# Kernel optimization log

Hardware: AMD Instinct MI355X
Metric: run time of the kernel (lower is better)

The kernel has to match this reference:

```python
import jax, jax.numpy as jnp
import numpy as np

N, E, B, DIM, NF, EF, HID = 50000, 100000, 2000, 64, 14, 4, 128


def setup_inputs() -> dict:
    key = jax.random.key(0)
    ks = jax.random.split(key, 30)
    rn = lambda k, shape, scale: jax.random.normal(k, shape, jnp.float32) * scale
    inp = {}
    inp["x"] = rn(ks[0], (N, NF), 1.0)
    inp["edge_attr"] = jax.random.uniform(ks[1], (E, EF), jnp.float32)
    inp["edge_index"] = jax.random.randint(ks[2], (2, E), 0, N)
    # equal-size graphs: 25 nodes per graph, sorted segment ids
    inp["batch"] = (jnp.arange(N, dtype=jnp.int32) // (N // B)).astype(jnp.int32)
    inp["lin0_w"] = rn(ks[3], (DIM, NF), (1.0 / NF) ** 0.5)
    inp["lin0_b"] = jnp.zeros((DIM,), jnp.float32)
    inp["mlp_w1"] = rn(ks[4], (HID, EF), (1.0 / EF) ** 0.5)
    inp["mlp_b1"] = jnp.zeros((HID,), jnp.float32)
    inp["mlp_w2"] = rn(ks[5], (DIM * DIM, HID), (1.0 / HID) ** 0.5)
    inp["mlp_b2"] = jnp.zeros((DIM * DIM,), jnp.float32)
    inp["root"] = rn(ks[6], (DIM, DIM), (1.0 / DIM) ** 0.5)
    inp["conv_b"] = jnp.zeros((DIM,), jnp.float32)
    inp["gru_wih"] = rn(ks[7], (3 * DIM, DIM), (1.0 / DIM) ** 0.5)
    inp["gru_whh"] = rn(ks[8], (3 * DIM, DIM), (1.0 / DIM) ** 0.5)
    inp["gru_bih"] = jnp.zeros((3 * DIM,), jnp.float32)
    inp["gru_bhh"] = jnp.zeros((3 * DIM,), jnp.float32)
    inp["lstm_wih"] = rn(ks[9], (4 * DIM, 2 * DIM), (1.0 / (2 * DIM)) ** 0.5)
    inp["lstm_whh"] = rn(ks[10], (4 * DIM, DIM), (1.0 / DIM) ** 0.5)
    inp["lstm_bih"] = jnp.zeros((4 * DIM,), jnp.float32)
    inp["lstm_bhh"] = jnp.zeros((4 * DIM,), jnp.float32)
    inp["lin1_w"] = rn(ks[11], (DIM, 2 * DIM), (1.0 / (2 * DIM)) ** 0.5)
    inp["lin1_b"] = jnp.zeros((DIM,), jnp.float32)
    inp["lin2_w"] = rn(ks[12], (1, DIM), (1.0 / DIM) ** 0.5)
    inp["lin2_b"] = jnp.zeros((1,), jnp.float32)
    return inp


def _forward(x, edge_attr, edge_index, batch, lin0_w, lin0_b, mlp_w1, mlp_b1,
             mlp_w2, mlp_b2, root, conv_b, gru_wih, gru_whh, gru_bih, gru_bhh,
             lstm_wih, lstm_whh, lstm_bih, lstm_bhh, lin1_w, lin1_b, lin2_w, lin2_b):
    src, dst = edge_index[0], edge_index[1]
    n = x.shape[0]
    # edge MLP -> per-edge weight matrices [E, DIM, DIM]
    h_e = jax.nn.relu(edge_attr @ mlp_w1.T + mlp_b1)
    W_e = (h_e @ mlp_w2.T + mlp_b2).reshape(-1, DIM, DIM)
    deg = jnp.clip(jax.ops.segment_sum(jnp.ones_like(dst, jnp.float32), dst, n), 1.0)

    out = jax.nn.relu(x @ lin0_w.T + lin0_b)
    h = out  # GRU hidden (seq_len=1, 1 layer)
    for _ in range(3):
        msg = jnp.einsum('ei,eio->eo', out[src], W_e)  # per-edge matmul
        agg = jax.ops.segment_sum(msg, dst, n) / deg[:, None]  # scatter-mean
        m = jax.nn.relu(agg + out @ root + conv_b)  # NNConv: aggr + root + bias
        # GRU step
        gi = m @ gru_wih.T + gru_bih
        gh = h @ gru_whh.T + gru_bhh
        i_r, i_z, i_n = jnp.split(gi, 3, axis=-1)
        h_r, h_z, h_n = jnp.split(gh, 3, axis=-1)
        r = jax.nn.sigmoid(i_r + h_r)
        z = jax.nn.sigmoid(i_z + h_z)
        ng = jnp.tanh(i_n + r * h_n)
        h = (1.0 - z) * ng + z * h
        out = h

    # Set2Set pooling, 3 processing steps
    b = B
    qh = jnp.zeros((b, DIM), out.dtype)
    qc = jnp.zeros((b, DIM), out.dtype)
    q_star = jnp.zeros((b, 2 * DIM), out.dtype)
    for _ in range(3):
        gates = q_star @ lstm_wih.T + lstm_bih + qh @ lstm_whh.T + lstm_bhh
        gi_, gf_, gg_, go_ = jnp.split(gates, 4, axis=-1)
        qc = jax.nn.sigmoid(gf_) * qc + jax.nn.sigmoid(gi_) * jnp.tanh(gg_)
        qh = jax.nn.sigmoid(go_) * jnp.tanh(qc)
        q = qh
        e = jnp.sum(out * q[batch], axis=-1)  # [N]
        e_max = jax.ops.segment_max(e, batch, b)
        a = jnp.exp(e - e_max[batch])
        denom = jax.ops.segment_sum(a, batch, b)
        a = a / denom[batch]
        r_read = jax.ops.segment_sum(a[:, None] * out, batch, b)
        q_star = jnp.concatenate([q, r_read], axis=-1)

    y = jax.nn.relu(q_star @ lin1_w.T + lin1_b)
    y = y @ lin2_w.T + lin2_b
    return y.reshape(-1)


def reference(x, edge_attr, edge_index, batch, lin0_w, lin0_b, mlp_w1, mlp_b1,
              mlp_w2, mlp_b2, root, conv_b, gru_wih, gru_whh, gru_bih, gru_bhh,
              lstm_wih, lstm_whh, lstm_bih, lstm_bhh, lin1_w, lin1_b, lin2_w, lin2_b):
    return _forward(x, edge_attr, edge_index, batch, lin0_w, lin0_b, mlp_w1, mlp_b1,
                    mlp_w2, mlp_b2, root, conv_b, gru_wih, gru_whh, gru_bih, gru_bhh,
                    lstm_wih, lstm_whh, lstm_bih, lstm_bhh, lin1_w, lin1_b, lin2_w, lin2_b)
```

## Files before the change

kernel.cpp:

```cpp
#include <hip/hip_runtime.h>
#include <hip/hip_bf16.h>

#define NN 50000
#define EE 100000
#define BB 2000
#define DIM 64
#define NF 14
#define EF 4
#define HID 128
#define EPAD 100096

typedef __attribute__((ext_vector_type(8))) _Float16 half8;
typedef __attribute__((ext_vector_type(4))) _Float16 half4;
typedef __attribute__((ext_vector_type(4))) float floatx4;

__device__ __forceinline__ float rcp_fast(float x) { return __builtin_amdgcn_rcpf(x); }
__device__ __forceinline__ float sig_fast(float x) { return rcp_fast(1.f + __expf(-x)); }
__device__ __forceinline__ float tanh_fast(float x) {
    float e = __expf(2.f * x);
    return 1.f - 2.f * rcp_fast(e + 1.f);
}

__global__ void prep_fused_kernel(
    const float* __restrict__ x, const float* __restrict__ lin0_w,
    const float* __restrict__ lin0_b, float* __restrict__ hv,
    const float* __restrict__ ea, const float* __restrict__ w1,
    const float* __restrict__ b1, _Float16* __restrict__ he,
    const int* __restrict__ ei, float* __restrict__ deg,
    const float* __restrict__ w2, _Float16* __restrict__ W2rT,
    const float* __restrict__ lih, const float* __restrict__ lhh,
    const float* __restrict__ l1, float* __restrict__ lihT,
    float* __restrict__ lhhT, float* __restrict__ l1T,
    const float* __restrict__ root, const float* __restrict__ b2,
    const float* __restrict__ gwih, const float* __restrict__ gwhh,
    const float* __restrict__ gbih, const float* __restrict__ gbhh,
    _Float16* __restrict__ W1h, _Float16* __restrict__ W2h,
    float* __restrict__ fbias) {
    int t = blockIdx.x * 256 + threadIdx.x;

    {
        int el = t >> 4, hc = t & 15;
        if (el < EPAD) {
            half8 o8 = {0, 0, 0, 0, 0, 0, 0, 0};
            if (el < EE) {
                const float4 a = *(const float4*)(ea + (size_t)el * 4);
                #pragma unroll
                for (int j = 0; j < 8; j++) {
                    int h = hc * 8 + j;
                    const float4 w = *(const float4*)(w1 + h * 4);
                    float acc = fmaxf(b1[h] + a.x * w.x + a.y * w.y + a.z * w.z + a.w * w.w, 0.f);
                    o8[j] = (_Float16)acc;
                }
                if (hc == 0) atomicAdd(&deg[ei[EE + el]], 1.0f);
            }
            *(half8*)(he + (size_t)el * 128 + hc * 8) = o8;
        }
    }
    if (t < NN * 8) {
        int n = t >> 3, dc = t & 7;
        float xv[NF];
        #pragma unroll
        for (int f = 0; f < NF; f++) xv[f] = x[(size_t)n * NF + f];
        float o[8];
        #pragma unroll
        for (int j = 0; j < 8; j++) {
            int d = dc * 8 + j;
            float acc = lin0_b[d];
            #pragma unroll
            for (int f = 0; f < NF; f++) acc += xv[f] * lin0_w[d * NF + f];
            o[j] = fmaxf(acc, 0.f);
        }
        *(float4*)(hv + (size_t)n * 64 + dc * 8)     = make_float4(o[0], o[1], o[2], o[3]);
        *(float4*)(hv + (size_t)n * 64 + dc * 8 + 4) = make_float4(o[4], o[5], o[6], o[7]);
    }
    if (t < 64 * 1024) {
        int o = t >> 10, kc = t & 1023;
        int k0 = kc * 8, i = k0 >> 7, h0 = k0 & 127;
        const float* src = w2 + (size_t)(i * 64 + o) * 128 + h0;
        const float4 a = *(const float4*)src;
        const float4 b = *(const float4*)(src + 4);
        half8 r = {(_Float16)a.x, (_Float16)a.y, (_Float16)a.z, (_Float16)a.w,
                   (_Float16)b.x, (_Float16)b.y, (_Float16)b.z, (_Float16)b.w};
        *(half8*)(W2rT + (size_t)o * 8192 + k0) = r;
    }
    if (t < 256 * 128) { int j = t / 128, k = t % 128; lihT[k * 256 + j] = lih[t]; }
    if (t < 256 * 64) { int j = t / 64, k = t % 64; lhhT[k * 256 + j] = lhh[t]; }
    if (t < 64 * 128) { int d = t / 128, k = t % 128; l1T[k * 64 + d] = l1[t]; }
    if (t < 64 * 128) {
        int n = t >> 7, k = t & 127;
        W1h[t] = (_Float16)(k < 64 ? root[k * 64 + n] : b2[(size_t)(k - 64) * 64 + n]);
    }
    if (t < 256 * 128) {
        int n2 = t >> 7, k = t & 127;
        int g = n2 >> 6, j = n2 & 63;
        float v;
        if (g == 0)      v = (k < 64) ? gwih[j * 64 + k]         : gwhh[j * 64 + (k - 64)];
        else if (g == 1) v = (k < 64) ? gwih[(64 + j) * 64 + k]  : gwhh[(64 + j) * 64 + (k - 64)];
        else if (g == 2) v = (k < 64) ? gwih[(128 + j) * 64 + k] : 0.f;
        else             v = (k < 64) ? 0.f                      : gwhh[(128 + j) * 64 + (k - 64)];
        W2h[t] = (_Float16)v;
    }
    if (t < 256) {
        int g = t >> 6, j = t & 63;
        float v = (g == 0) ? gbih[j] + gbhh[j]
                : (g == 1) ? gbih[64 + j] + gbhh[64 + j]
                : (g == 2) ? gbih[128 + j] : gbhh[128 + j];
        fbias[t] = v;
    }
}

__global__ __launch_bounds__(256, 2) void msg_gemm_kernel(
    const float* __restrict__ hv, const _Float16* __restrict__ he16,
    const _Float16* __restrict__ W2rT, const int* __restrict__ ei,
    float* __restrict__ agg, float* __restrict__ xsum) {
    __shared__ _Float16 sB[2][16 * 64 * 8];
    __shared__ _Float16 sXs[256 * 68];
    __shared__ int sDst[256];
    const int t = threadIdx.x;
    const int tile = blockIdx.x >> 1;
    const int ki = blockIdx.x & 1;
    const int eb = tile * 256;
    const int base = ki * 32;
    const int lane = t & 63;
    const int w = t >> 6;
    const int col = lane & 15;
    const int quad = lane >> 4;

    if (t < 256) {
        int e = eb + t;
        sDst[t] = (e < EE) ? ei[EE + e] : 0;
    }
    if (ki == 0) {
        #pragma unroll 4
        for (int rep = 0; rep < 16; rep++) {
            int idx = rep * 256 + t;
            int el = idx >> 4, d4 = idx & 15;
            int e = eb + el;
            float4 v = {0.f, 0.f, 0.f, 0.f};
            if (e < EE) {
                int src = ei[e];
                v = *(const float4*)(hv + (size_t)src * 64 + d4 * 4);
            }
            half4 h4 = {(_Float16)v.x, (_Float16)v.y, (_Float16)v.z, (_Float16)v.w};
            *(half4*)&sXs[el * 68 + d4 * 4] = h4;
        }
    } else {
        #pragma unroll 4
        for (int rep = 0; rep < 8; rep++) {
            int idx = rep * 256 + t;
            int el = idx >> 3, d4 = 8 + (idx & 7);
            int e = eb + el;
            float4 v = {0.f, 0.f, 0.f, 0.f};
            if (e < EE) {
                int src = ei[e];
                v = *(const float4*)(hv + (size_t)src * 64 + d4 * 4);
            }
            half4 h4 = {(_Float16)v.x, (_Float16)v.y, (_Float16)v.z, (_Float16)v.w};
            *(half4*)&sXs[el * 68 + d4 * 4] = h4;
        }
    }

    half8 heReg[4][4];
    #pragma unroll
    for (int mt = 0; mt < 4; mt++) {
        int row = eb + w * 64 + mt * 16 + col;
        #pragma unroll
        for (int p = 0; p < 4; p++)
            heReg[mt][p] = *(const half8*)(he16 + (size_t)row * 128 + p * 32 + quad * 8);
    }

    floatx4 Cacc[4][4];
    #pragma unroll
    for (int mt = 0; mt < 4; mt++)
        #pragma unroll
        for (int nt = 0; nt < 4; nt++)
            Cacc[mt][nt] = (floatx4){0.f, 0.f, 0.f, 0.f};

    const size_t gbase = (size_t)(w * 16 + col) * 8192 + quad * 8;
    half8 pre[4];
    {
        #pragma unroll
        for (int rep = 0; rep < 4; rep++)
            pre[rep] = *(const half8*)(W2rT + gbase + (size_t)base * 128 + rep * 32);
        #pragma unroll
        for (int rep = 0; rep < 4; rep++)
            *(half8*)&sB[0][((w * 4 + rep) * 64 + lane) * 8] = pre[rep];
    }
    __syncthreads();

    #pragma unroll 1
    for (int ii = 0; ii < 32; ii++) {
        int buf = ii & 1;
        if (ii < 31) {
            #pragma unroll
            for (int rep = 0; rep < 4; rep++)
                pre[rep] = *(const half8*)(W2rT + gbase + (size_t)(base + ii + 1) * 128 + rep * 32);
        }
        _Float16 xsx[4];
        #pragma unroll
        for (int mt = 0; mt < 4; mt++)
            xsx[mt] = sXs[(w * 64 + mt * 16 + col) * 68 + base + ii];
        #pragma unroll
        for (int ks = 0; ks < 4; ks++) {
            half8 bfr[4];
            #pragma unroll
            for (int nt = 0; nt < 4; nt++)
                bfr[nt] = *(const half8*)&sB[buf][((nt * 4 + ks) * 64 + lane) * 8];
            #pragma unroll
            for (int mt = 0; mt < 4; mt++) {
                half8 afr = heReg[mt][ks] * xsx[mt];
                #pragma unroll
                for (int nt = 0; nt < 4; nt++)
                    Cacc[mt][nt] = __builtin_amdgcn_mfma_f32_16x16x32_f16(afr, bfr[nt], Cacc[mt][nt], 0, 0, 0);
            }
        }
        if (ii < 31) {
            #pragma unroll
            for (int rep = 0; rep < 4; rep++)
                *(half8*)&sB[buf ^ 1][((w * 4 + rep) * 64 + lane) * 8] = pre[rep];
        }
        __syncthreads();
    }

    #pragma unroll
    for (int mt = 0; mt < 4; mt++) {
        #pragma unroll
        for (int r = 0; r < 4; r++) {
            int el = w * 64 + mt * 16 + quad * 4 + r;
            if (eb + el < EE) {
                float* ap = agg + (size_t)sDst[el] * 64 + col;
                #pragma unroll
                for (int nt = 0; nt < 4; nt++)
                    atomicAdd(ap + nt * 16, Cacc[mt][nt][r]);
            }
        }
    }
    if (ki == 0) {
        #pragma unroll 4
        for (int rep = 0; rep < 64; rep++) {
            int idx = rep * 256 + t;
            int el = idx >> 6, d = idx & 63;
            if (eb + el < EE)
                atomicAdd(&xsum[(size_t)sDst[el] * 64 + d], (float)sXs[el * 68 + d]);
        }
    }
}

__global__ __launch_bounds__(256, 2) void node_fused_kernel(
    const float* __restrict__ hv_in, float* __restrict__ agg,
    float* __restrict__ xsum, const float* __restrict__ deg,
    const _Float16* __restrict__ W1h, const _Float16* __restrict__ W2h,
    const float* __restrict__ fbias, const float* __restrict__ cb,
    float* __restrict__ hv_out) {
    __shared__ _Float16 sA1[64 * 136];
    __shared__ _Float16 sA2[64 * 136];
    __shared__ float sH[64 * 68];
    __shared__ float sAgg[64 * 68];
    const int t = threadIdx.x;
    const int nb = blockIdx.x * 64;
    const int n = t >> 2, part = t & 3;
    {
        int gn = nb + n;
        bool valid = gn < NN;
        float inv = 1.f;
        if (valid) inv = 1.f / fmaxf(deg[gn], 1.f);
        #pragma unroll
        for (int c4 = 0; c4 < 4; c4++) {
            int d0 = part * 16 + c4 * 4;
            float4 hvv = {0.f, 0.f, 0.f, 0.f}, agv = {0.f, 0.f, 0.f, 0.f}, xsv = {0.f, 0.f, 0.f, 0.f};
            if (valid) {
                hvv = *(const float4*)(hv_in + (size_t)gn * 64 + d0);
                agv = *(const float4*)(agg + (size_t)gn * 64 + d0);
                xsv = *(const float4*)(xsum + (size_t)gn * 64 + d0);
            }
            agv.x *= inv; agv.y *= inv; agv.z *= inv; agv.w *= inv;
            xsv.x *= inv; xsv.y *= inv; xsv.z *= inv; xsv.w *= inv;
            half4 hvh = {(_Float16)hvv.x, (_Float16)hvv.y, (_Float16)hvv.z, (_Float16)hvv.w};
            half4 xsh = {(_Float16)xsv.x, (_Float16)xsv.y, (_Float16)xsv.z, (_Float16)xsv.w};
            *(half4*)&sA1[n * 136 + d0] = hvh;
            *(half4*)&sA1[n * 136 + 64 + d0] = xsh;
            *(half4*)&sA2[n * 136 + 64 + d0] = hvh;
            *(float4*)&sH[n * 68 + d0] = hvv;
            *(float4*)&sAgg[n * 68 + d0] = agv;
        }
        if (valid) {
            float4 z = {0.f, 0.f, 0.f, 0.f};
            #pragma unroll
            for (int c4 = 0; c4 < 4; c4++) {
                int d0 = part * 16 + c4 * 4;
                *(float4*)(agg + (size_t)gn * 64 + d0) = z;
                *(float4*)(xsum + (size_t)gn * 64 + d0) = z;
            }
        }
    }
    __syncthreads();

    const int lane = t & 63, w = t >> 6;
    const int col = lane & 15, quad = lane >> 4;

    floatx4 C1[4];
    #pragma unroll
    for (int nt = 0; nt < 4; nt++) {
        float b = cb[nt * 16 + col];
        C1[nt] = (floatx4){b, b, b, b};
    }
    #pragma unroll
    for (int ks = 0; ks < 4; ks++) {
        half8 a = *(const half8*)&sA1[(w * 16 + col) * 136 + ks * 32 + quad * 8];
        #pragma unroll
        for (int nt = 0; nt < 4; nt++) {
            half8 bfr = *(const half8*)(W1h + (size_t)(nt * 16 + col) * 128 + ks * 32 + quad * 8);
            C1[nt] = __builtin_amdgcn_mfma_f32_16x16x32_f16(a, bfr, C1[nt], 0, 0, 0);
        }
    }
    #pragma unroll
    for (int nt = 0; nt < 4; nt++) {
        #pragma unroll
        for (int r = 0; r < 4; r++) {
            int node = w * 16 + quad * 4 + r;
            int j = nt * 16 + col;
            float m = fmaxf(C1[nt][r] + sAgg[node * 68 + j], 0.f);
            sA2[node * 136 + j] = (_Float16)m;
        }
    }
    __syncthreads();

    floatx4 C2[16];
    #pragma unroll
    for (int nt2 = 0; nt2 < 16; nt2++) {
        float b = fbias[nt2 * 16 + col];
        C2[nt2] = (floatx4){b, b, b, b};
    }
    #pragma unroll
    for (int ks = 0; ks < 4; ks++) {
        half8 a = *(const half8*)&sA2[(w * 16 + col) * 136 + ks * 32 + quad * 8];
        #pragma unroll
        for (int nt2 = 0; nt2 < 16; nt2++) {
            half8 bfr = *(const half8*)(W2h + (size_t)(nt2 * 16 + col) * 128 + ks * 32 + quad * 8);
            C2[nt2] = __builtin_amdgcn_mfma_f32_16x16x32_f16(a, bfr, C2[nt2], 0, 0, 0);
        }
    }
    float hnew[4][4];
    #pragma unroll
    for (int r = 0; r < 4; r++) {
        int node = w * 16 + quad * 4 + r;
        #pragma unroll
        for (int jt = 0; jt < 4; jt++) {
            int j = jt * 16 + col;
            float rr = sig_fast(C2[jt][r]);
            float zz = sig_fast(C2[4 + jt][r]);
            float ng = tanh_fast(C2[8 + jt][r] + rr * C2[12 + jt][r]);
            float hold = sH[node * 68 + j];
            hnew[r][jt] = (1.f - zz) * ng + zz * hold;
        }
    }
    __syncthreads();
    #pragma unroll
    for (int r = 0; r < 4; r++) {
        int node = w * 16 + quad * 4 + r;
        #pragma unroll
        for (int jt = 0; jt < 4; jt++)
            sH[node * 68 + jt * 16 + col] = hnew[r][jt];
    }
    __syncthreads();
    {
        int gn = nb + n;
        if (gn < NN) {
            #pragma unroll
            for (int c4 = 0; c4 < 4; c4++) {
                int d0 = part * 16 + c4 * 4;
                *(float4*)(hv_out + (size_t)gn * 64 + d0) = *(const float4*)&sH[n * 68 + d0];
            }
        }
    }
}

__global__ __launch_bounds__(256) void set2set_kernel(
    const float* __restrict__ hv,
    const float* __restrict__ lihT, const float* __restrict__ lhhT,
    const float* __restrict__ l_bih, const float* __restrict__ l_bhh,
    const float* __restrict__ lin1T, const float* __restrict__ lin1_b,
    const float* __restrict__ lin2_w, const float* __restrict__ lin2_b,
    float* __restrict__ out) {
    __shared__ float outS[25 * 65];
    __shared__ float qs[128], qh[64], qc[64], gat[256], ew[32], aw[32], red[64];
    int g = blockIdx.x;
    int t = threadIdx.x;
    for (int p = t; p < 25 * 64; p += 256) {
        int j = p >> 6, i = p & 63;
        outS[j * 65 + i] = hv[(size_t)(g * 25 + j) * 64 + i];
    }
    if (t < 128) qs[t] = 0.f;
    if (t < 64) { qh[t] = 0.f; qc[t] = 0.f; }
    __syncthreads();
    for (int it = 0; it < 3; it++) {
        float acc = l_bih[t] + l_bhh[t];
        for (int k = 0; k < 128; k++) acc += qs[k] * lihT[k * 256 + t];
        for (int k = 0; k < 64; k++) acc += qh[k] * lhhT[k * 256 + t];
        gat[t] = acc;
        __syncthreads();
        if (t < 64) {
            float ig = sig_fast(gat[t]);
            float fg = sig_fast(gat[64 + t]);
            float gg = tanh_fast(gat[128 + t]);
            float og = sig_fast(gat[192 + t]);
            float c = fg * qc[t] + ig * gg;
            qc[t] = c;
            qh[t] = og * tanh_fast(c);
        }
        __syncthreads();
        if (t < 25) {
            float e = 0.f;
            for (int i = 0; i < 64; i++) e += outS[t * 65 + i] * qh[i];
            ew[t] = e;
        }
        __syncthreads();
        if (t == 0) {
            float mx = ew[0];
            for (int j = 1; j < 25; j++) mx = fmaxf(mx, ew[j]);
            float s = 0.f;
            for (int j = 0; j < 25; j++) { float a = __expf(ew[j] - mx); aw[j] = a; s += a; }
            float inv = rcp_fast(s);
            for (int j = 0; j < 25; j++) aw[j] *= inv;
        }
        __syncthreads();
        if (t < 64) {
            float r = 0.f;
            for (int j = 0; j < 25; j++) r += aw[j] * outS[j * 65 + t];
            qs[t] = qh[t];
            qs[64 + t] = r;
        }
        __syncthreads();
    }
    if (t < 64) {
        float y1 = lin1_b[t];
        for (int k = 0; k < 128; k++) y1 += qs[k] * lin1T[k * 64 + t];
        y1 = fmaxf(y1, 0.f);
        red[t] = y1 * lin2_w[t];
    }
    __syncthreads();
    if (t == 0) {
        float y = lin2_b[0];
        for (int i = 0; i < 64; i++) y += red[i];
        out[g] = y;
    }
}

extern "C" void kernel_launch(void* const* d_in, const int* in_sizes, int n_in,
                              void* d_out, int out_size, void* d_ws, size_t ws_size,
                              hipStream_t stream) {
    const float* x        = (const float*)d_in[0];
    const float* ea       = (const float*)d_in[1];
    const int*   ei       = (const int*)  d_in[2];
    const float* lin0_w   = (const float*)d_in[4];
    const float* lin0_b   = (const float*)d_in[5];
    const float* mlp_w1   = (const float*)d_in[6];
    const float* mlp_b1   = (const float*)d_in[7];
    const float* mlp_w2   = (const float*)d_in[8];
    const float* mlp_b2   = (const float*)d_in[9];
    const float* root     = (const float*)d_in[10];
    const float* conv_b   = (const float*)d_in[11];
    const float* gru_wih  = (const float*)d_in[12];
    const float* gru_whh  = (const float*)d_in[13];
    const float* gru_bih  = (const float*)d_in[14];
    const float* gru_bhh  = (const float*)d_in[15];
    const float* lstm_wih = (const float*)d_in[16];
    const float* lstm_whh = (const float*)d_in[17];
    const float* lstm_bih = (const float*)d_in[18];
    const float* lstm_bhh = (const float*)d_in[19];
    const float* lin1_w   = (const float*)d_in[20];
    const float* lin1_b   = (const float*)d_in[21];
    const float* lin2_w   = (const float*)d_in[22];
    const float* lin2_b   = (const float*)d_in[23];
    float* out = (float*)d_out;

    char* base = (char*)d_ws;
    size_t off = 0;
    auto carve = [&](size_t bytes) -> void* {
        void* r = base + off;
        off = (off + bytes + 255) & ~(size_t)255;
        return r;
    };
    float* hv   = (float*)carve((size_t)NN * 64 * 4);
    float* agg  = (float*)carve((size_t)NN * 64 * 4);
    float* xsum = (float*)carve((size_t)NN * 64 * 4);
    float* deg  = (float*)carve((size_t)NN * 4);
    float* lihT = (float*)carve(128 * 256 * 4);
    float* lhhT = (float*)carve(64 * 256 * 4);
    float* l1T  = (float*)carve(128 * 64 * 4);
    float* fbias = (float*)carve(256 * 4);
    _Float16* he16 = (_Float16*)carve((size_t)EPAD * 128 * 2);
    _Float16* W2rT = (_Float16*)carve((size_t)64 * 8192 * 2);
    _Float16* W1h  = (_Float16*)carve((size_t)64 * 128 * 2);
    _Float16* W2h  = (_Float16*)carve((size_t)256 * 128 * 2);

    hipMemsetAsync(agg, 0, (size_t)NN * 64 * 4 * 2 + (size_t)NN * 4, stream);
    prep_fused_kernel<<<EPAD * 16 / 256, 256, 0, stream>>>(
        x, lin0_w, lin0_b, hv,
        ea, mlp_w1, mlp_b1, he16, ei, deg,
        mlp_w2, W2rT,
        lstm_wih, lstm_whh, lin1_w, lihT, lhhT, l1T,
        root, mlp_b2, gru_wih, gru_whh, gru_bih, gru_bhh,
        W1h, W2h, fbias);

    for (int it = 0; it < 3; it++) {
        msg_gemm_kernel<<<(EPAD / 256) * 2, 256, 0, stream>>>(hv, he16, W2rT, ei, agg, xsum);
        node_fused_kernel<<<(NN + 63) / 64, 256, 0, stream>>>(hv, agg, xsum, deg,
                                                              W1h, W2h, fbias, conv_b, hv);
    }

    set2set_kernel<<<BB, 256, 0, stream>>>(hv, lihT, lhhT, lstm_bih, lstm_bhh,
                                           l1T, lin1_b, lin2_w, lin2_b, out);
}
```

Before: 812.5 us.

## Drop K-split in message GEMM and add 512-edge tile variant for first iteration

The message GEMM no longer splits the 64-wide reduction across two blocks per edge tile. Each block now loops over all 64 K slices, so every edge tile is gathered once and its xsum scatter is done by one block. A second kernel that processes 512 edges per block with eight M-tiles per wave is used for the first iteration only, to get more reuse of the streamed W2 tiles. The costs are half as many blocks in flight, higher register pressure in the 512-edge variant (launch bounds of 1), and a longer serial K loop per block.

```diff
diff --git a/kernel.cpp b/kernel.cpp
--- a/kernel.cpp
+++ b/kernel.cpp
@@ -9,6 +9,7 @@
 #define EF 4
 #define HID 128
 #define EPAD 100096
+#define EPAD2 100352
 
 typedef __attribute__((ext_vector_type(8))) _Float16 half8;
 typedef __attribute__((ext_vector_type(4))) _Float16 half4;
@@ -40,7 +41,7 @@
 
     {
         int el = t >> 4, hc = t & 15;
-        if (el < EPAD) {
+        if (el < EPAD2) {
             half8 o8 = {0, 0, 0, 0, 0, 0, 0, 0};
             if (el < EE) {
                 const float4 a = *(const float4*)(ea + (size_t)el * 4);
@@ -117,10 +118,7 @@
     __shared__ _Float16 sXs[256 * 68];
     __shared__ int sDst[256];
     const int t = threadIdx.x;
-    const int tile = blockIdx.x >> 1;
-    const int ki = blockIdx.x & 1;
-    const int eb = tile * 256;
-    const int base = ki * 32;
+    const int eb = blockIdx.x * 256;
     const int lane = t & 63;
     const int w = t >> 6;
     const int col = lane & 15;
@@ -130,34 +128,18 @@
         int e = eb + t;
         sDst[t] = (e < EE) ? ei[EE + e] : 0;
     }
-    if (ki == 0) {
-        #pragma unroll 4
-        for (int rep = 0; rep < 16; rep++) {
-            int idx = rep * 256 + t;
-            int el = idx >> 4, d4 = idx & 15;
-            int e = eb + el;
-            float4 v = {0.f, 0.f, 0.f, 0.f};
-            if (e < EE) {
-                int src = ei[e];
-                v = *(const float4*)(hv + (size_t)src * 64 + d4 * 4);
-            }
-            half4 h4 = {(_Float16)v.x, (_Float16)v.y, (_Float16)v.z, (_Float16)v.w};
-            *(half4*)&sXs[el * 68 + d4 * 4] = h4;
-        }
-    } else {
-        #pragma unroll 4
-        for (int rep = 0; rep < 8; rep++) {
-            int idx = rep * 256 + t;
-            int el = idx >> 3, d4 = 8 + (idx & 7);
-            int e = eb + el;
-            float4 v = {0.f, 0.f, 0.f, 0.f};
-            if (e < EE) {
-                int src = ei[e];
-                v = *(const float4*)(hv + (size_t)src * 64 + d4 * 4);
-            }
-            half4 h4 = {(_Float16)v.x, (_Float16)v.y, (_Float16)v.z, (_Float16)v.w};
-            *(half4*)&sXs[el * 68 + d4 * 4] = h4;
-        }
+    #pragma unroll 4
+    for (int rep = 0; rep < 16; rep++) {
+        int idx = rep * 256 + t;
+        int el = idx >> 4, d4 = idx & 15;
+        int e = eb + el;
+        float4 v = {0.f, 0.f, 0.f, 0.f};
+        if (e < EE) {
+            int src = ei[e];
+            v = *(const float4*)(hv + (size_t)src * 64 + d4 * 4);
+        }
+        half4 h4 = {(_Float16)v.x, (_Float16)v.y, (_Float16)v.z, (_Float16)v.w};
+        *(half4*)&sXs[el * 68 + d4 * 4] = h4;
     }
 
     half8 heReg[4][4];
@@ -181,7 +163,7 @@
     {
         #pragma unroll
         for (int rep = 0; rep < 4; rep++)
-            pre[rep] = *(const half8*)(W2rT + gbase + (size_t)base * 128 + rep * 32);
+            pre[rep] = *(const half8*)(W2rT + gbase + 0 * 128 + rep * 32);
         #pragma unroll
         for (int rep = 0; rep < 4; rep++)
             *(half8*)&sB[0][((w * 4 + rep) * 64 + lane) * 8] = pre[rep];
@@ -189,17 +171,17 @@
     __syncthreads();
 
     #pragma unroll 1
-    for (int ii = 0; ii < 32; ii++) {
-        int buf = ii & 1;
-        if (ii < 31) {
+    for (int i = 0; i < 64; i++) {
+        int buf = i & 1;
+        if (i < 63) {
             #pragma unroll
             for (int rep = 0; rep < 4; rep++)
-                pre[rep] = *(const half8*)(W2rT + gbase + (size_t)(base + ii + 1) * 128 + rep * 32);
+                pre[rep] = *(const half8*)(W2rT + gbase + (size_t)(i + 1) * 128 + rep * 32);
         }
         _Float16 xsx[4];
         #pragma unroll
         for (int mt = 0; mt < 4; mt++)
-            xsx[mt] = sXs[(w * 64 + mt * 16 + col) * 68 + base + ii];
+            xsx[mt] = sXs[(w * 64 + mt * 16 + col) * 68 + i];
         #pragma unroll
         for (int ks = 0; ks < 4; ks++) {
             half8 bfr[4];
@@ -214,7 +196,7 @@
                     Cacc[mt][nt] = __builtin_amdgcn_mfma_f32_16x16x32_f16(afr, bfr[nt], Cacc[mt][nt], 0, 0, 0);
             }
         }
-        if (ii < 31) {
+        if (i < 63) {
             #pragma unroll
             for (int rep = 0; rep < 4; rep++)
                 *(half8*)&sB[buf ^ 1][((w * 4 + rep) * 64 + lane) * 8] = pre[rep];
@@ -235,14 +217,130 @@
             }
         }
     }
-    if (ki == 0) {
-        #pragma unroll 4
-        for (int rep = 0; rep < 64; rep++) {
-            int idx = rep * 256 + t;
-            int el = idx >> 6, d = idx & 63;
-            if (eb + el < EE)
-                atomicAdd(&xsum[(size_t)sDst[el] * 64 + d], (float)sXs[el * 68 + d]);
-        }
+    #pragma unroll 4
+    for (int rep = 0; rep < 64; rep++) {
+        int idx = rep * 256 + t;
+        int el = idx >> 6, d = idx & 63;
+        if (eb + el < EE)
+            atomicAdd(&xsum[(size_t)sDst[el] * 64 + d], (float)sXs[el * 68 + d]);
+    }
+}
+
+__global__ __launch_bounds__(256, 1) void msg_gemm2_kernel(
+    const float* __restrict__ hv, const _Float16* __restrict__ he16,
+    const _Float16* __restrict__ W2rT, const int* __restrict__ ei,
+    float* __restrict__ agg, float* __restrict__ xsum) {
+    __shared__ _Float16 sB[2][16 * 64 * 8];
+    __shared__ _Float16 sXs[512 * 68];
+    __shared__ int sDst[512];
+    const int t = threadIdx.x;
+    const int eb = blockIdx.x * 512;
+    const int lane = t & 63;
+    const int w = t >> 6;
+    const int col = lane & 15;
+    const int quad = lane >> 4;
+
+    #pragma unroll
+    for (int rep = 0; rep < 2; rep++) {
+        int idx = rep * 256 + t;
+        int e = eb + idx;
+        sDst[idx] = (e < EE) ? ei[EE + e] : 0;
+    }
+    #pragma unroll 4
+    for (int rep = 0; rep < 32; rep++) {
+        int idx = rep * 256 + t;
+        int el = idx >> 4, d4 = idx & 15;
+        int e = eb + el;
+        float4 v = {0.f, 0.f, 0.f, 0.f};
+        if (e < EE) {
+            int src = ei[e];
+            v = *(const float4*)(hv + (size_t)src * 64 + d4 * 4);
+        }
+        half4 h4 = {(_Float16)v.x, (_Float16)v.y, (_Float16)v.z, (_Float16)v.w};
+        *(half4*)&sXs[el * 68 + d4 * 4] = h4;
+    }
+
+    half8 heReg[8][4];
+    #pragma unroll
+    for (int mt = 0; mt < 8; mt++) {
+        int row = eb + w * 128 + mt * 16 + col;
+        #pragma unroll
+        for (int p = 0; p < 4; p++)
+            heReg[mt][p] = *(const half8*)(he16 + (size_t)row * 128 + p * 32 + quad * 8);
+    }
+
+    floatx4 Cacc[8][4];
+    #pragma unroll
+    for (int mt = 0; mt < 8; mt++)
+        #pragma unroll
+        for (int nt = 0; nt < 4; nt++)
+            Cacc[mt][nt] = (floatx4){0.f, 0.f, 0.f, 0.f};
+
+    const size_t gbase = (size_t)(w * 16 + col) * 8192 + quad * 8;
+    half8 pre[4];
+    {
+        #pragma unroll
+        for (int rep = 0; rep < 4; rep++)
+            pre[rep] = *(const half8*)(W2rT + gbase + 0 * 128 + rep * 32);
+        #pragma unroll
+        for (int rep = 0; rep < 4; rep++)
+            *(half8*)&sB[0][((w * 4 + rep) * 64 + lane) * 8] = pre[rep];
+    }
+    __syncthreads();
+
+    #pragma unroll 1
+    for (int i = 0; i < 64; i++) {
+        int buf = i & 1;
+        if (i < 63) {
+            #pragma unroll
+            for (int rep = 0; rep < 4; rep++)
+                pre[rep] = *(const half8*)(W2rT + gbase + (size_t)(i + 1) * 128 + rep * 32);
+        }
+        _Float16 xsx[8];
+        #pragma unroll
+        for (int mt = 0; mt < 8; mt++)
+            xsx[mt] = sXs[(w * 128 + mt * 16 + col) * 68 + i];
+        #pragma unroll
+        for (int ks = 0; ks < 4; ks++) {
+            half8 bfr[4];
+            #pragma unroll
+            for (int nt = 0; nt < 4; nt++)
+                bfr[nt] = *(const half8*)&sB[buf][((nt * 4 + ks) * 64 + lane) * 8];
+            #pragma unroll
+            for (int mt = 0; mt < 8; mt++) {
+                half8 afr = heReg[mt][ks] * xsx[mt];
+                #pragma unroll
+                for (int nt = 0; nt < 4; nt++)
+                    Cacc[mt][nt] = __builtin_amdgcn_mfma_f32_16x16x32_f16(afr, bfr[nt], Cacc[mt][nt], 0, 0, 0);
+            }
+        }
+        if (i < 63) {
+            #pragma unroll
+            for (int rep = 0; rep < 4; rep++)
+                *(half8*)&sB[buf ^ 1][((w * 4 + rep) * 64 + lane) * 8] = pre[rep];
+        }
+        __syncthreads();
+    }
+
+    #pragma unroll
+    for (int mt = 0; mt < 8; mt++) {
+        #pragma unroll
+        for (int r = 0; r < 4; r++) {
+            int el = w * 128 + mt * 16 + quad * 4 + r;
+            if (eb + el < EE) {
+                float* ap = agg + (size_t)sDst[el] * 64 + col;
+                #pragma unroll
+                for (int nt = 0; nt < 4; nt++)
+                    atomicAdd(ap + nt * 16, Cacc[mt][nt][r]);
+            }
+        }
+    }
+    #pragma unroll 4
+    for (int rep = 0; rep < 128; rep++) {
+        int idx = rep * 256 + t;
+        int el = idx >> 6, d = idx & 63;
+        if (eb + el < EE)
+            atomicAdd(&xsum[(size_t)sDst[el] * 64 + d], (float)sXs[el * 68 + d]);
     }
 }
 
@@ -489,13 +587,13 @@
     float* lhhT = (float*)carve(64 * 256 * 4);
     float* l1T  = (float*)carve(128 * 64 * 4);
     float* fbias = (float*)carve(256 * 4);
-    _Float16* he16 = (_Float16*)carve((size_t)EPAD * 128 * 2);
+    _Float16* he16 = (_Float16*)carve((size_t)EPAD2 * 128 * 2);
     _Float16* W2rT = (_Float16*)carve((size_t)64 * 8192 * 2);
     _Float16* W1h  = (_Float16*)carve((size_t)64 * 128 * 2);
     _Float16* W2h  = (_Float16*)carve((size_t)256 * 128 * 2);
 
     hipMemsetAsync(agg, 0, (size_t)NN * 64 * 4 * 2 + (size_t)NN * 4, stream);
-    prep_fused_kernel<<<EPAD * 16 / 256, 256, 0, stream>>>(
+    prep_fused_kernel<<<EPAD2 * 16 / 256, 256, 0, stream>>>(
         x, lin0_w, lin0_b, hv,
         ea, mlp_w1, mlp_b1, he16, ei, deg,
         mlp_w2, W2rT,
@@ -504,7 +602,10 @@
         W1h, W2h, fbias);
 
     for (int it = 0; it < 3; it++) {
-        msg_gemm_kernel<<<(EPAD / 256) * 2, 256, 0, stream>>>(hv, he16, W2rT, ei, agg, xsum);
+        if (it == 0)
+            msg_gemm2_kernel<<<EPAD2 / 512, 256, 0, stream>>>(hv, he16, W2rT, ei, agg, xsum);
+        else
+            msg_gemm_kernel<<<EPAD / 256, 256, 0, stream>>>(hv, he16, W2rT, ei, agg, xsum);
         node_fused_kernel<<<(NN + 63) / 64, 256, 0, stream>>>(hv, agg, xsum, deg,
                                                               W1h, W2h, fbias, conv_b, hv);
     }
```

New measurement: 768.5 us. -5.4%, faster.

## Drop split-K in message GEMM and write GRU output directly from registers

Applied to the files above, without the earlier changes.

The message GEMM no longer splits the 64-wide source-feature reduction across two blocks per edge tile. Each block now gathers all features and runs the full 64-step loop, which halves the atomic adds into agg and removes the duplicated gather. The trade-off is half as many blocks, which may leave compute units underused. It also raises wave priority around the MFMA section. In the node kernel the sH staging buffer and its two barriers are removed: GRU outputs go straight from registers to global, reading the old state from global, and the launch bound is raised to 3 blocks per CU.

```diff
diff --git a/kernel.cpp b/kernel.cpp
--- a/kernel.cpp
+++ b/kernel.cpp
@@ -9,6 +9,7 @@
 #define EF 4
 #define HID 128
 #define EPAD 100096
+#define EPAD2 100352
 
 typedef __attribute__((ext_vector_type(8))) _Float16 half8;
 typedef __attribute__((ext_vector_type(4))) _Float16 half4;
@@ -40,7 +41,7 @@
 
     {
         int el = t >> 4, hc = t & 15;
-        if (el < EPAD) {
+        if (el < EPAD2) {
             half8 o8 = {0, 0, 0, 0, 0, 0, 0, 0};
             if (el < EE) {
                 const float4 a = *(const float4*)(ea + (size_t)el * 4);
@@ -117,10 +118,7 @@
     __shared__ _Float16 sXs[256 * 68];
     __shared__ int sDst[256];
     const int t = threadIdx.x;
-    const int tile = blockIdx.x >> 1;
-    const int ki = blockIdx.x & 1;
-    const int eb = tile * 256;
-    const int base = ki * 32;
+    const int eb = blockIdx.x * 256;
     const int lane = t & 63;
     const int w = t >> 6;
     const int col = lane & 15;
@@ -130,34 +128,18 @@
         int e = eb + t;
         sDst[t] = (e < EE) ? ei[EE + e] : 0;
     }
-    if (ki == 0) {
-        #pragma unroll 4
-        for (int rep = 0; rep < 16; rep++) {
-            int idx = rep * 256 + t;
-            int el = idx >> 4, d4 = idx & 15;
-            int e = eb + el;
-            float4 v = {0.f, 0.f, 0.f, 0.f};
-            if (e < EE) {
-                int src = ei[e];
-                v = *(const float4*)(hv + (size_t)src * 64 + d4 * 4);
-            }
-            half4 h4 = {(_Float16)v.x, (_Float16)v.y, (_Float16)v.z, (_Float16)v.w};
-            *(half4*)&sXs[el * 68 + d4 * 4] = h4;
-        }
-    } else {
-        #pragma unroll 4
-        for (int rep = 0; rep < 8; rep++) {
-            int idx = rep * 256 + t;
-            int el = idx >> 3, d4 = 8 + (idx & 7);
-            int e = eb + el;
-            float4 v = {0.f, 0.f, 0.f, 0.f};
-            if (e < EE) {
-                int src = ei[e];
-                v = *(const float4*)(hv + (size_t)src * 64 + d4 * 4);
-            }
-            half4 h4 = {(_Float16)v.x, (_Float16)v.y, (_Float16)v.z, (_Float16)v.w};
-            *(half4*)&sXs[el * 68 + d4 * 4] = h4;
-        }
+    #pragma unroll 4
+    for (int rep = 0; rep < 16; rep++) {
+        int idx = rep * 256 + t;
+        int el = idx >> 4, d4 = idx & 15;
+        int e = eb + el;
+        float4 v = {0.f, 0.f, 0.f, 0.f};
+        if (e < EE) {
+            int src = ei[e];
+            v = *(const float4*)(hv + (size_t)src * 64 + d4 * 4);
+        }
+        half4 h4 = {(_Float16)v.x, (_Float16)v.y, (_Float16)v.z, (_Float16)v.w};
+        *(half4*)&sXs[el * 68 + d4 * 4] = h4;
     }
 
     half8 heReg[4][4];
@@ -181,7 +163,7 @@
     {
         #pragma unroll
         for (int rep = 0; rep < 4; rep++)
-            pre[rep] = *(const half8*)(W2rT + gbase + (size_t)base * 128 + rep * 32);
+            pre[rep] = *(const half8*)(W2rT + gbase + 0 * 128 + rep * 32);
         #pragma unroll
         for (int rep = 0; rep < 4; rep++)
             *(half8*)&sB[0][((w * 4 + rep) * 64 + lane) * 8] = pre[rep];
@@ -189,17 +171,18 @@
     __syncthreads();
 
     #pragma unroll 1
-    for (int ii = 0; ii < 32; ii++) {
-        int buf = ii & 1;
-        if (ii < 31) {
+    for (int i = 0; i < 64; i++) {
+        int buf = i & 1;
+        if (i < 63) {
             #pragma unroll
             for (int rep = 0; rep < 4; rep++)
-                pre[rep] = *(const half8*)(W2rT + gbase + (size_t)(base + ii + 1) * 128 + rep * 32);
+                pre[rep] = *(const half8*)(W2rT + gbase + (size_t)(i + 1) * 128 + rep * 32);
         }
         _Float16 xsx[4];
         #pragma unroll
         for (int mt = 0; mt < 4; mt++)
-            xsx[mt] = sXs[(w * 64 + mt * 16 + col) * 68 + base + ii];
+            xsx[mt] = sXs[(w * 64 + mt * 16 + col) * 68 + i];
+        __builtin_amdgcn_s_setprio(1);
         #pragma unroll
         for (int ks = 0; ks < 4; ks++) {
             half8 bfr[4];
@@ -214,7 +197,8 @@
                     Cacc[mt][nt] = __builtin_amdgcn_mfma_f32_16x16x32_f16(afr, bfr[nt], Cacc[mt][nt], 0, 0, 0);
             }
         }
-        if (ii < 31) {
+        __builtin_amdgcn_s_setprio(0);
+        if (i < 63) {
             #pragma unroll
             for (int rep = 0; rep < 4; rep++)
                 *(half8*)&sB[buf ^ 1][((w * 4 + rep) * 64 + lane) * 8] = pre[rep];
@@ -235,18 +219,16 @@
             }
         }
     }
-    if (ki == 0) {
-        #pragma unroll 4
-        for (int rep = 0; rep < 64; rep++) {
-            int idx = rep * 256 + t;
-            int el = idx >> 6, d = idx & 63;
-            if (eb + el < EE)
-                atomicAdd(&xsum[(size_t)sDst[el] * 64 + d], (float)sXs[el * 68 + d]);
-        }
-    }
-}
-
-__global__ __launch_bounds__(256, 2) void node_fused_kernel(
+    #pragma unroll 4
+    for (int rep = 0; rep < 64; rep++) {
+        int idx = rep * 256 + t;
+        int el = idx >> 6, d = idx & 63;
+        if (eb + el < EE)
+            atomicAdd(&xsum[(size_t)sDst[el] * 64 + d], (float)sXs[el * 68 + d]);
+    }
+}
+
+__global__ __launch_bounds__(256, 3) void node_fused_kernel(
     const float* __restrict__ hv_in, float* __restrict__ agg,
     float* __restrict__ xsum, const float* __restrict__ deg,
     const _Float16* __restrict__ W1h, const _Float16* __restrict__ W2h,
@@ -254,7 +236,6 @@
     float* __restrict__ hv_out) {
     __shared__ _Float16 sA1[64 * 136];
     __shared__ _Float16 sA2[64 * 136];
-    __shared__ float sH[64 * 68];
     __shared__ float sAgg[64 * 68];
     const int t = threadIdx.x;
     const int nb = blockIdx.x * 64;
@@ -280,7 +261,6 @@
             *(half4*)&sA1[n * 136 + d0] = hvh;
             *(half4*)&sA1[n * 136 + 64 + d0] = xsh;
             *(half4*)&sA2[n * 136 + 64 + d0] = hvh;
-            *(float4*)&sH[n * 68 + d0] = hvv;
             *(float4*)&sAgg[n * 68 + d0] = agv;
         }
         if (valid) {
@@ -340,36 +320,19 @@
             C2[nt2] = __builtin_amdgcn_mfma_f32_16x16x32_f16(a, bfr, C2[nt2], 0, 0, 0);
         }
     }
-    float hnew[4][4];
     #pragma unroll
     for (int r = 0; r < 4; r++) {
         int node = w * 16 + quad * 4 + r;
-        #pragma unroll
-        for (int jt = 0; jt < 4; jt++) {
-            int j = jt * 16 + col;
-            float rr = sig_fast(C2[jt][r]);
-            float zz = sig_fast(C2[4 + jt][r]);
-            float ng = tanh_fast(C2[8 + jt][r] + rr * C2[12 + jt][r]);
-            float hold = sH[node * 68 + j];
-            hnew[r][jt] = (1.f - zz) * ng + zz * hold;
-        }
-    }
-    __syncthreads();
-    #pragma unroll
-    for (int r = 0; r < 4; r++) {
-        int node = w * 16 + quad * 4 + r;
-        #pragma unroll
-        for (int jt = 0; jt < 4; jt++)
-            sH[node * 68 + jt * 16 + col] = hnew[r][jt];
-    }
-    __syncthreads();
-    {
-        int gn = nb + n;
-        if (gn < NN) {
-            #pragma unroll
-            for (int c4 = 0; c4 < 4; c4++) {
-                int d0 = part * 16 + c4 * 4;
-                *(float4*)(hv_out + (size_t)gn * 64 + d0) = *(const float4*)&sH[n * 68 + d0];
+        int gn2 = nb + node;
+        if (gn2 < NN) {
+            #pragma unroll
+            for (int jt = 0; jt < 4; jt++) {
+                int j = jt * 16 + col;
+                float rr = sig_fast(C2[jt][r]);
+                float zz = sig_fast(C2[4 + jt][r]);
+                float ng = tanh_fast(C2[8 + jt][r] + rr * C2[12 + jt][r]);
+                float hold = hv_in[(size_t)gn2 * 64 + j];
+                hv_out[(size_t)gn2 * 64 + j] = (1.f - zz) * ng + zz * hold;
             }
         }
     }
@@ -489,13 +452,13 @@
     float* lhhT = (float*)carve(64 * 256 * 4);
     float* l1T  = (float*)carve(128 * 64 * 4);
     float* fbias = (float*)carve(256 * 4);
-    _Float16* he16 = (_Float16*)carve((size_t)EPAD * 128 * 2);
+    _Float16* he16 = (_Float16*)carve((size_t)EPAD2 * 128 * 2);
     _Float16* W2rT = (_Float16*)carve((size_t)64 * 8192 * 2);
     _Float16* W1h  = (_Float16*)carve((size_t)64 * 128 * 2);
     _Float16* W2h  = (_Float16*)carve((size_t)256 * 128 * 2);
 
     hipMemsetAsync(agg, 0, (size_t)NN * 64 * 4 * 2 + (size_t)NN * 4, stream);
-    prep_fused_kernel<<<EPAD * 16 / 256, 256, 0, stream>>>(
+    prep_fused_kernel<<<EPAD2 * 16 / 256, 256, 0, stream>>>(
         x, lin0_w, lin0_b, hv,
         ea, mlp_w1, mlp_b1, he16, ei, deg,
         mlp_w2, W2rT,
@@ -504,7 +467,7 @@
         W1h, W2h, fbias);
 
     for (int it = 0; it < 3; it++) {
-        msg_gemm_kernel<<<(EPAD / 256) * 2, 256, 0, stream>>>(hv, he16, W2rT, ei, agg, xsum);
+        msg_gemm_kernel<<<EPAD / 256, 256, 0, stream>>>(hv, he16, W2rT, ei, agg, xsum);
         node_fused_kernel<<<(NN + 63) / 64, 256, 0, stream>>>(hv, agg, xsum, deg,
                                                               W1h, W2h, fbias, conv_b, hv);
     }
```

After: 731.9 us. 1.11x faster.
